# Optimization experiments

Measured on AMD Instinct MI355X. Metric: run time of the kernel, lower is better.

Reference implementation:

```python
import jax, jax.numpy as jnp
import numpy as np

HZ, TAU1, TAU2, TSCALE = 20.0, 0.5, 0.05, 6.0

def _double_exp_kernel(hz, tau1, tau2, tscale):
    # Faithful to SpikeToCalcium.set_double_exp (tau1 > tau2 assumed)
    t1 = tau1 * hz
    t2 = tau2 * hz
    r = t1 / t2
    d = t1 - t2
    scale = np.power(r, -t2 / d) - np.power(r, -t1 / d)
    t = np.arange(1.0, t1 * tscale + 2.0, dtype=np.float32)
    return ((np.exp(-t / t1) - np.exp(-t / t2)) / scale).astype(np.float32)  # size 61

def setup_inputs() -> dict:
    key = jax.random.key(0)
    u = jax.random.uniform(key, (1024, 30000), dtype=jnp.float32)  # [cells, T] spike activity
    kernel = jnp.asarray(_double_exp_kernel(HZ, TAU1, TAU2, TSCALE))  # [K]=61
    return {"u": u, "kernel": kernel}

def reference(u, kernel):
    # Keras: conv1d(u[...,None], kernel[::-1], 'valid'); tf conv = cross-correlation,
    # so with the reversed kernel this is a true causal FIR convolution.
    krev = kernel[::-1]
    out = jax.lax.conv_general_dilated(
        u[:, None, :],              # [N, 1, T]
        krev[None, None, :],        # [O=1, I=1, K]
        window_strides=(1,),
        padding='VALID',
    )  # [N, 1, T-K+1]
    return out[:, 0, :]
```

## Files before the change

### kernel.cpp

```cpp
#include <hip/hip_runtime.h>

#define K_TAPS   61
#define R_OUT    7
#define BLOCK    256
#define TILE_OUT (BLOCK * R_OUT)
#define TILE_IN  (TILE_OUT + K_TAPS - 1)

__global__ __launch_bounds__(BLOCK)
void SpikeToCalcium_conv1d_kernel(const float* __restrict__ u,
                                  const float* __restrict__ kern,
                                  float* __restrict__ out,
                                  int L, int M, long long total_in)
{
    __shared__ float sx[TILE_IN];
    __shared__ float sk[K_TAPS];

    const int t          = threadIdx.x;
    const int row        = blockIdx.y;
    const int tile_start = blockIdx.x * TILE_OUT;

    if (t < K_TAPS) sk[t] = kern[K_TAPS - 1 - t];

    const long long gbase = (long long)row * L + tile_start;
    for (int v = t; v < TILE_IN / 4; v += BLOCK) {
        const long long g = gbase + 4LL * v;
        float4 val;
        if (g + 3 < total_in) {
            val = *reinterpret_cast<const float4*>(u + g);
        } else {
            val.x = (g + 0 < total_in) ? u[g + 0] : 0.0f;
            val.y = (g + 1 < total_in) ? u[g + 1] : 0.0f;
            val.z = (g + 2 < total_in) ? u[g + 2] : 0.0f;
            val.w = (g + 3 < total_in) ? u[g + 3] : 0.0f;
        }
        *reinterpret_cast<float4*>(sx + 4 * v) = val;
    }
    __syncthreads();

    const int off = t * R_OUT;

    float acc[R_OUT];
    float w[R_OUT];
#pragma unroll
    for (int r = 0; r < R_OUT; ++r) acc[r] = 0.0f;
#pragma unroll
    for (int r = 0; r < R_OUT; ++r) w[r] = sx[off + r];

#pragma unroll
    for (int k = 0; k < K_TAPS; ++k) {
        const float kv = sk[k];
#pragma unroll
        for (int r = 0; r < R_OUT; ++r) acc[r] = fmaf(w[r], kv, acc[r]);
        if (k < K_TAPS - 1) {
#pragma unroll
            for (int r = 0; r < R_OUT - 1; ++r) w[r] = w[r + 1];
            w[R_OUT - 1] = sx[off + k + R_OUT];
        }
    }

    const long long orow = (long long)row * M;
    const int nbase = tile_start + off;
#pragma unroll
    for (int r = 0; r < R_OUT; ++r) {
        const int n = nbase + r;
        if (n < M) out[orow + n] = acc[r];
    }
}

extern "C" void kernel_launch(void* const* d_in, const int* in_sizes, int n_in,
                              void* d_out, int out_size, void* d_ws, size_t ws_size,
                              hipStream_t stream) {
    const float* u    = (const float*)d_in[0];
    const float* kern = (const float*)d_in[1];
    float*       out  = (float*)d_out;

    const long long total_in = (long long)in_sizes[0];
    const int ROWS = (int)((total_in - (long long)out_size) / (K_TAPS - 1));
    const int L    = (int)(total_in / ROWS);
    const int M    = L - K_TAPS + 1;

    const int blocks_per_row = (M + TILE_OUT - 1) / TILE_OUT;
    dim3 grid(blocks_per_row, ROWS);
    SpikeToCalcium_conv1d_kernel<<<grid, BLOCK, 0, stream>>>(
        u, kern, out, L, M, total_in);
}
```

Measured before the change: 261.7 us.

## Replace shared-memory tiling with per-thread register windows and vectorized stores

Removes the LDS staging tile and the __syncthreads barrier. Each thread now loads its own 76-float input window straight from global memory into registers with float4 loads, reads the filter taps directly from global memory, and computes 16 outputs per thread instead of 7. Outputs are written with float4 stores when the thread's 16 outputs are fully in range. This is meant to cut LDS traffic and register shuffling in the FMA loop, at the cost of overlapping, strided per-thread global reads that depend on L1/L2 hits, plus higher register pressure. The float4 path also assumes 16-byte alignment of the row offsets.

```diff
diff --git a/kernel.cpp b/kernel.cpp
--- a/kernel.cpp
+++ b/kernel.cpp
@@ -1,10 +1,10 @@
 #include <hip/hip_runtime.h>
 
 #define K_TAPS   61
-#define R_OUT    7
+#define R_OUT    16
 #define BLOCK    256
 #define TILE_OUT (BLOCK * R_OUT)
-#define TILE_IN  (TILE_OUT + K_TAPS - 1)
+#define WIN      (R_OUT + K_TAPS - 1)
 
 __global__ __launch_bounds__(BLOCK)
 void SpikeToCalcium_conv1d_kernel(const float* __restrict__ u,
@@ -12,58 +12,51 @@
                                   float* __restrict__ out,
                                   int L, int M, long long total_in)
 {
-    __shared__ float sx[TILE_IN];
-    __shared__ float sk[K_TAPS];
+    const int t    = threadIdx.x;
+    const int row  = blockIdx.y;
+    const int base = blockIdx.x * TILE_OUT + t * R_OUT;
+    if (base >= M) return;
 
-    const int t          = threadIdx.x;
-    const int row        = blockIdx.y;
-    const int tile_start = blockIdx.x * TILE_OUT;
+    const long long g = (long long)row * L + base;
 
-    if (t < K_TAPS) sk[t] = kern[K_TAPS - 1 - t];
-
-    const long long gbase = (long long)row * L + tile_start;
-    for (int v = t; v < TILE_IN / 4; v += BLOCK) {
-        const long long g = gbase + 4LL * v;
-        float4 val;
-        if (g + 3 < total_in) {
-            val = *reinterpret_cast<const float4*>(u + g);
-        } else {
-            val.x = (g + 0 < total_in) ? u[g + 0] : 0.0f;
-            val.y = (g + 1 < total_in) ? u[g + 1] : 0.0f;
-            val.z = (g + 2 < total_in) ? u[g + 2] : 0.0f;
-            val.w = (g + 3 < total_in) ? u[g + 3] : 0.0f;
+    float w[WIN];
+    if (g + WIN <= total_in) {
+#pragma unroll
+        for (int i = 0; i < WIN / 4; ++i) {
+            const float4 v = *reinterpret_cast<const float4*>(u + g + 4 * i);
+            w[4 * i + 0] = v.x; w[4 * i + 1] = v.y;
+            w[4 * i + 2] = v.z; w[4 * i + 3] = v.w;
         }
-        *reinterpret_cast<float4*>(sx + 4 * v) = val;
+    } else {
+#pragma unroll
+        for (int i = 0; i < WIN; ++i)
+            w[i] = (g + i < total_in) ? u[g + i] : 0.0f;
     }
-    __syncthreads();
-
-    const int off = t * R_OUT;
 
     float acc[R_OUT];
-    float w[R_OUT];
 #pragma unroll
     for (int r = 0; r < R_OUT; ++r) acc[r] = 0.0f;
-#pragma unroll
-    for (int r = 0; r < R_OUT; ++r) w[r] = sx[off + r];
 
 #pragma unroll
     for (int k = 0; k < K_TAPS; ++k) {
-        const float kv = sk[k];
+        const float kv = kern[K_TAPS - 1 - k];
 #pragma unroll
-        for (int r = 0; r < R_OUT; ++r) acc[r] = fmaf(w[r], kv, acc[r]);
-        if (k < K_TAPS - 1) {
-#pragma unroll
-            for (int r = 0; r < R_OUT - 1; ++r) w[r] = w[r + 1];
-            w[R_OUT - 1] = sx[off + k + R_OUT];
-        }
+        for (int r = 0; r < R_OUT; ++r)
+            acc[r] = fmaf(w[r + k], kv, acc[r]);
     }
 
-    const long long orow = (long long)row * M;
-    const int nbase = tile_start + off;
+    const long long o = (long long)row * M + base;
+    if (base + R_OUT <= M) {
 #pragma unroll
-    for (int r = 0; r < R_OUT; ++r) {
-        const int n = nbase + r;
-        if (n < M) out[orow + n] = acc[r];
+        for (int i = 0; i < R_OUT / 4; ++i) {
+            const float4 v = make_float4(acc[4 * i + 0], acc[4 * i + 1],
+                                         acc[4 * i + 2], acc[4 * i + 3]);
+            *reinterpret_cast<float4*>(out + o + 4 * i) = v;
+        }
+    } else {
+#pragma unroll
+        for (int r = 0; r < R_OUT; ++r)
+            if (base + r < M) out[o + r] = acc[r];
     }
 }
 
```

Result: no change. 262.6 us (+0.3%).

## Restructure FIR conv to float4 shared-memory windows, scalar taps, vector stores

Applied to the files above, without the earlier changes.

Drops outputs per thread from 7 to 4 and has each thread read its 64-sample input window from shared memory as 16 float4 loads instead of a scalar sliding register window. Filter taps are now read directly from global memory with uniform, compile-time indices, which can go through the scalar path, so the shared-memory kernel copy is removed. Each thread writes its 4 outputs with one float4 store, giving contiguous, coalesced writes instead of the previous stride-7 pattern. The cost is fewer outputs per thread (less register reuse) and more blocks per row.

```diff
diff --git a/kernel.cpp b/kernel.cpp
--- a/kernel.cpp
+++ b/kernel.cpp
@@ -1,10 +1,13 @@
 #include <hip/hip_runtime.h>
 
 #define K_TAPS   61
-#define R_OUT    7
+#define R_OUT    4
 #define BLOCK    256
 #define TILE_OUT (BLOCK * R_OUT)
 #define TILE_IN  (TILE_OUT + K_TAPS - 1)
+#define TILE_IN4 ((TILE_IN + 3) / 4)
+#define WIN      (R_OUT + K_TAPS - 1)
+#define NV       (WIN / 4)
 
 __global__ __launch_bounds__(BLOCK)
 void SpikeToCalcium_conv1d_kernel(const float* __restrict__ u,
@@ -12,17 +15,15 @@
                                   float* __restrict__ out,
                                   int L, int M, long long total_in)
 {
-    __shared__ float sx[TILE_IN];
-    __shared__ float sk[K_TAPS];
+    __shared__ float sx[TILE_IN4 * 4];
 
     const int t          = threadIdx.x;
     const int row        = blockIdx.y;
     const int tile_start = blockIdx.x * TILE_OUT;
 
-    if (t < K_TAPS) sk[t] = kern[K_TAPS - 1 - t];
-
     const long long gbase = (long long)row * L + tile_start;
-    for (int v = t; v < TILE_IN / 4; v += BLOCK) {
+    float4* sxv = reinterpret_cast<float4*>(sx);
+    for (int v = t; v < TILE_IN4; v += BLOCK) {
         const long long g = gbase + 4LL * v;
         float4 val;
         if (g + 3 < total_in) {
@@ -33,37 +34,37 @@
             val.z = (g + 2 < total_in) ? u[g + 2] : 0.0f;
             val.w = (g + 3 < total_in) ? u[g + 3] : 0.0f;
         }
-        *reinterpret_cast<float4*>(sx + 4 * v) = val;
+        sxv[v] = val;
     }
     __syncthreads();
 
-    const int off = t * R_OUT;
-
-    float acc[R_OUT];
-    float w[R_OUT];
-#pragma unroll
-    for (int r = 0; r < R_OUT; ++r) acc[r] = 0.0f;
-#pragma unroll
-    for (int r = 0; r < R_OUT; ++r) w[r] = sx[off + r];
+    float acc[R_OUT] = {0.0f, 0.0f, 0.0f, 0.0f};
 
 #pragma unroll
-    for (int k = 0; k < K_TAPS; ++k) {
-        const float kv = sk[k];
+    for (int i = 0; i < NV; ++i) {
+        const float4 x = sxv[t + i];
+        const float xs[4] = {x.x, x.y, x.z, x.w};
 #pragma unroll
-        for (int r = 0; r < R_OUT; ++r) acc[r] = fmaf(w[r], kv, acc[r]);
-        if (k < K_TAPS - 1) {
+        for (int j = 0; j < 4; ++j) {
+            const int p = 4 * i + j;
 #pragma unroll
-            for (int r = 0; r < R_OUT - 1; ++r) w[r] = w[r + 1];
-            w[R_OUT - 1] = sx[off + k + R_OUT];
+            for (int r = 0; r < R_OUT; ++r) {
+                const int k = p - r;
+                if (k >= 0 && k < K_TAPS)
+                    acc[r] = fmaf(xs[j], kern[K_TAPS - 1 - k], acc[r]);
+            }
         }
     }
 
-    const long long orow = (long long)row * M;
-    const int nbase = tile_start + off;
+    const int obase = tile_start + 4 * t;
+    const long long o = (long long)row * M + obase;
+    if (obase + R_OUT <= M) {
+        *reinterpret_cast<float4*>(out + o) =
+            make_float4(acc[0], acc[1], acc[2], acc[3]);
+    } else {
 #pragma unroll
-    for (int r = 0; r < R_OUT; ++r) {
-        const int n = nbase + r;
-        if (n < M) out[orow + n] = acc[r];
+        for (int r = 0; r < R_OUT; ++r)
+            if (obase + r < M) out[o + r] = acc[r];
     }
 }
 
```

Measured after the change: 293.4 us. 12.1% more time.
